# Kernel tuning notes

Measured on AMD Instinct MI355X. Metric: run time of the kernel, lower is better.

## Reference

```python
import jax, jax.numpy as jnp
import numpy as np

silu = jax.nn.silu

B, N, E, H, T, L, A = 8, 20000, 40000, 128, 64, 4, 4


def setup_inputs() -> dict:
    key = jax.random.key(0)
    ks = jax.random.split(key, 20)
    s = 0.05
    w = lambda k, shape: jax.random.normal(k, shape, jnp.float32) * s
    return {
        "x": jax.random.normal(ks[0], (B, N, 3), jnp.float32),
        "t": jax.random.uniform(ks[1], (B,), jnp.float32) * 1000.0,
        "atom_types": jax.random.randint(ks[2], (N,), 0, A),
        "bond_indices": jax.random.randint(ks[3], (E, 2), 0, N),
        "emb_table": w(ks[4], (A, H)),
        "W_t1": w(ks[5], (T, H)), "b_t1": jnp.zeros((H,), jnp.float32),
        "W_t2": w(ks[6], (H, H)), "b_t2": jnp.zeros((H,), jnp.float32),
        "W_node": w(ks[7], (H, H)), "b_node": jnp.zeros((H,), jnp.float32),
        "Wm1": w(ks[8], (L, 2 * H + 1, H)), "bm1": jnp.zeros((L, H), jnp.float32),
        "Wm2": w(ks[9], (L, H, H)), "bm2": jnp.zeros((L, H), jnp.float32),
        "Wn1": w(ks[10], (L, 2 * H, H)), "bn1": jnp.zeros((L, H), jnp.float32),
        "Wn2": w(ks[11], (L, H, H)), "bn2": jnp.zeros((L, H), jnp.float32),
        "Wc1": w(ks[12], (L, H, H)), "bc1": jnp.zeros((L, H), jnp.float32),
        "Wc2": w(ks[13], (L, H, 1)) * 0.001,  # xavier gain=0.001 final coord layer
        "W_o1": w(ks[14], (H, H)), "b_o1": jnp.zeros((H,), jnp.float32),
        "W_o2": w(ks[15], (H, 3)), "b_o2": jnp.zeros((3,), jnp.float32),
    }


def reference(x, t, atom_types, bond_indices, emb_table,
              W_t1, b_t1, W_t2, b_t2, W_node, b_node,
              Wm1, bm1, Wm2, bm2, Wn1, bn1, Wn2, bn2, Wc1, bc1, Wc2,
              W_o1, b_o1, W_o2, b_o2):
    n_atoms = x.shape[1]
    src = bond_indices[:, 0]
    dst = bond_indices[:, 1]

    # sinusoidal time embedding -> time MLP
    half = W_t1.shape[0] // 2
    freq = jnp.exp(jnp.arange(half, dtype=jnp.float32) * (-np.log(10000.0) / (half - 1)))
    te = t[:, None] * freq[None, :]
    te = jnp.concatenate([jnp.sin(te), jnp.cos(te)], axis=-1)  # [B, T]
    t_emb = silu(te @ W_t1 + b_t1) @ W_t2 + b_t2  # [B, H]

    # node init: embedding -> linear -> + time emb
    h0 = emb_table[atom_types] @ W_node + b_node  # [N, H]
    h = h0[None, :, :] + t_emb[:, None, :]  # [B, N, H]

    # degree counts (src+dst incidence), clamped to >=1
    ones = jnp.ones((src.shape[0],), jnp.float32)
    counts = jnp.zeros((n_atoms,), jnp.float32).at[dst].add(ones).at[src].add(ones)
    counts = jnp.maximum(counts, 1.0)

    x_orig = x
    n_layers = Wm1.shape[0]
    for l in range(n_layers):
        h_src = h[:, src, :]
        h_dst = h[:, dst, :]
        coord_diff = x[:, dst, :] - x[:, src, :]  # [B, E, 3]
        dist = jnp.sqrt(jnp.sum(coord_diff * coord_diff, axis=-1, keepdims=True))
        msg_in = jnp.concatenate([h_src, h_dst, dist], axis=-1)  # [B, E, 2H+1]
        m = silu(msg_in @ Wm1[l] + bm1[l])
        m = silu(m @ Wm2[l] + bm2[l])  # [B, E, H]

        agg = jnp.zeros_like(h).at[:, dst, :].add(m).at[:, src, :].add(m)
        h_in = jnp.concatenate([h, agg], axis=-1)
        h = h + silu(h_in @ Wn1[l] + bn1[l]) @ Wn2[l] + bn2[l]

        cw = silu(m @ Wc1[l] + bc1[l]) @ Wc2[l]  # [B, E, 1]
        cdn = coord_diff / (dist + 1e-8)
        upd = cdn * cw
        coord_update = jnp.zeros_like(x).at[:, dst, :].add(upd).at[:, src, :].add(-upd)
        x = x + coord_update / counts[None, :, None]

    coord_change = x - x_orig
    noise_from_h = silu(h @ W_o1 + b_o1) @ W_o2 + b_o2
    return coord_change + noise_from_h
```

## Files before the change

### kernel.cpp

```cpp
#include <hip/hip_runtime.h>
#include <math.h>

#define B_ 8
#define N_ 20000
#define E_ 40000
#define H_ 128
#define L_ 4
#define A_ 4
#define TS 132
#define MRS 136
#define EPB 64
#define NPB 64

#define WFENCE __asm__ __volatile__("" ::: "memory")

typedef _Float16 f16x8 __attribute__((ext_vector_type(8)));
typedef _Float16 f16x4v __attribute__((ext_vector_type(4)));
typedef float f32x4 __attribute__((ext_vector_type(4)));

__device__ __forceinline__ float silu_f(float x) {
    return x * __builtin_amdgcn_rcpf(1.f + __expf(-x));
}


__global__ void k_zero(int* __restrict__ deg, int* __restrict__ cursor) {
    int i = blockIdx.x * 256 + threadIdx.x;
    if (i < N_) { deg[i] = 0; cursor[i] = 0; }
}

__global__ void k_deg(const int* __restrict__ bond, int* __restrict__ deg) {
    int e = blockIdx.x * 256 + threadIdx.x;
    if (e < E_) {
        atomicAdd(&deg[bond[2 * e]], 1);
        atomicAdd(&deg[bond[2 * e + 1]], 1);
    }
}

__global__ void k_scan(const int* __restrict__ deg, int* __restrict__ indptr) {
    __shared__ int sums[1024];
    const int CH = (N_ + 1023) / 1024;
    int t = threadIdx.x;
    int s0 = t * CH;
    int s1 = min(s0 + CH, N_);
    int s = 0;
    for (int i = s0; i < s1; ++i) s += deg[i];
    sums[t] = s;
    __syncthreads();
    for (int off = 1; off < 1024; off <<= 1) {
        int v = (t >= off) ? sums[t - off] : 0;
        __syncthreads();
        sums[t] += v;
        __syncthreads();
    }
    int base = (t > 0) ? sums[t - 1] : 0;
    int run = base;
    for (int i = s0; i < s1; ++i) { indptr[i] = run; run += deg[i]; }
    if (s1 == N_ && s0 < N_) indptr[N_] = run;
}

__global__ void k_fill(const int* __restrict__ bond, const int* __restrict__ indptr,
                       int* __restrict__ cursor, int* __restrict__ adj) {
    int e = blockIdx.x * 256 + threadIdx.x;
    if (e < E_) {
        int s = bond[2 * e], d = bond[2 * e + 1];
        int ps = indptr[s] + atomicAdd(&cursor[s], 1);
        adj[ps] = (e << 1);
        int pd = indptr[d] + atomicAdd(&cursor[d], 1);
        adj[pd] = (e << 1) | 1;
    }
}

__global__ void k_wprepL(const float* __restrict__ W, _Float16* __restrict__ Wf,
                         int K, int wstride) {
    int l = blockIdx.y;
    const float* Wl = W + (size_t)l * wstride;
    _Float16* Wfl = Wf + (size_t)l * K * 128;
    int idx = blockIdx.x * 256 + threadIdx.x;
    if (idx >= K * 128) return;
    int j = idx & 7, lane = (idx >> 3) & 63, nt = (idx >> 9) & 7, kt = idx >> 12;
    int k = kt * 32 + (lane >> 4) * 8 + j;
    int n = nt * 16 + (lane & 15);
    Wfl[idx] = (_Float16)Wl[k * 128 + n];
}

__global__ void k_temb(const float* __restrict__ tv,
                       const float* __restrict__ W1, const float* __restrict__ b1,
                       const float* __restrict__ W2, const float* __restrict__ b2,
                       float* __restrict__ t_emb) {
    __shared__ float te[64];
    __shared__ float h1[128];
    int b = blockIdx.x;
    int tid = threadIdx.x;
    float tval = tv[b];
    if (tid < 32) {
        float fr = __expf((float)tid * (-logf(10000.f) / 31.f));
        float a = tval * fr;
        te[tid] = sinf(a);
        te[tid + 32] = cosf(a);
    }
    __syncthreads();
    float acc = b1[tid];
    for (int k = 0; k < 64; ++k) acc += te[k] * W1[k * 128 + tid];
    h1[tid] = silu_f(acc);
    __syncthreads();
    float acc2 = b2[tid];
    for (int k = 0; k < 128; ++k) acc2 += h1[k] * W2[k * 128 + tid];
    t_emb[b * 128 + tid] = acc2;
}

__global__ void k_embproj(const float* __restrict__ emb, const float* __restrict__ W,
                          const float* __restrict__ bias, float* __restrict__ outp) {
    int tid = threadIdx.x;
    int a = tid >> 7, j = tid & 127;
    float acc = bias[j];
    for (int k = 0; k < 128; ++k) acc += emb[a * 128 + k] * W[k * 128 + j];
    outp[a * 128 + j] = acc;
}

__global__ void k_hinit(const int* __restrict__ at, const float* __restrict__ embp,
                        const float* __restrict__ temb, float* __restrict__ h,
                        _Float16* __restrict__ h16) {
    size_t idx4 = (size_t)blockIdx.x * 256 + threadIdx.x;
    size_t e0 = idx4 * 4;
    int j = (int)(e0 % H_);
    size_t bn = e0 / H_;
    int n = (int)(bn % N_);
    int b = (int)(bn / N_);
    int a = at[n];
    float4 ep = *(const float4*)(embp + a * H_ + j);
    float4 tv = *(const float4*)(temb + b * H_ + j);
    float4 r = make_float4(ep.x + tv.x, ep.y + tv.y, ep.z + tv.z, ep.w + tv.w);
    ((float4*)h)[idx4] = r;
    f16x4v o;
    o[0] = (_Float16)r.x; o[1] = (_Float16)r.y; o[2] = (_Float16)r.z; o[3] = (_Float16)r.w;
    *(f16x4v*)(h16 + e0) = o;
}

__global__ void k_xcopy(const float* __restrict__ x, float* __restrict__ xb) {
    int i = blockIdx.x * 256 + threadIdx.x;
    xb[i] = x[i];
}

template <int RS, int KT>
__device__ __forceinline__ void mfma_gemm(const _Float16* Asw, const _Float16* __restrict__ Wf,
                                          f32x4 (&acc)[8], int ml, int quad, int lane) {
    #pragma unroll
    for (int kt = 0; kt < KT; ++kt) {
        f16x8 a = *(const f16x8*)(Asw + ml * RS + kt * 32 + quad * 8);
        #pragma unroll
        for (int nt = 0; nt < 8; ++nt) {
            f16x8 b = *(const f16x8*)(Wf + (((kt * 8 + nt) * 64 + lane) * 8));
            acc[nt] = __builtin_amdgcn_mfma_f32_16x16x32_f16(a, b, acc[nt], 0, 0, 0);
        }
    }
}

template <int RS, int KT>
__device__ __forceinline__ void mfma_gemm2(const _Float16* Asw, const _Float16* __restrict__ Wf,
                                           f32x4 (&acc)[2][8], int ml, int quad, int lane) {
    #pragma unroll
    for (int kt = 0; kt < KT; ++kt) {
        f16x8 a0 = *(const f16x8*)(Asw + ml * RS + kt * 32 + quad * 8);
        f16x8 a1 = *(const f16x8*)(Asw + (16 + ml) * RS + kt * 32 + quad * 8);
        #pragma unroll
        for (int nt = 0; nt < 8; ++nt) {
            f16x8 b = *(const f16x8*)(Wf + (((kt * 8 + nt) * 64 + lane) * 8));
            acc[0][nt] = __builtin_amdgcn_mfma_f32_16x16x32_f16(a0, b, acc[0][nt], 0, 0, 0);
            acc[1][nt] = __builtin_amdgcn_mfma_f32_16x16x32_f16(a1, b, acc[1][nt], 0, 0, 0);
        }
    }
}

template <int STRIDE, int K>
__device__ __forceinline__ void gemm_t(const float* As, const float* __restrict__ W,
                                       float (&acc)[4][8], int r4, int c) {
    const float4* Wv = (const float4*)W;
    #pragma unroll 2
    for (int k = 0; k < K; k += 4) {
        float a[4][4];
        #pragma unroll
        for (int i = 0; i < 4; ++i)
            *(float4*)a[i] = *(const float4*)(As + (r4 + i) * STRIDE + k);
        #pragma unroll
        for (int kk = 0; kk < 4; ++kk) {
            float4 w0 = Wv[(k + kk) * 32 + c * 2];
            float4 w1 = Wv[(k + kk) * 32 + c * 2 + 1];
            #pragma unroll
            for (int i = 0; i < 4; ++i) {
                float av = a[i][kk];
                acc[i][0] += av * w0.x; acc[i][1] += av * w0.y;
                acc[i][2] += av * w0.z; acc[i][3] += av * w0.w;
                acc[i][4] += av * w1.x; acc[i][5] += av * w1.y;
                acc[i][6] += av * w1.z; acc[i][7] += av * w1.w;
            }
        }
    }
}

__device__ __forceinline__ void bias_init(float (&acc)[4][8], const float* __restrict__ bias, int c) {
    float4 b0 = ((const float4*)bias)[c * 2];
    float4 b1 = ((const float4*)bias)[c * 2 + 1];
    #pragma unroll
    for (int i = 0; i < 4; ++i) {
        acc[i][0] = b0.x; acc[i][1] = b0.y; acc[i][2] = b0.z; acc[i][3] = b0.w;
        acc[i][4] = b1.x; acc[i][5] = b1.y; acc[i][6] = b1.z; acc[i][7] = b1.w;
    }
}


__global__ __launch_bounds__(128, 4) void k_edge_mfma(
    const _Float16* __restrict__ h16, const float* __restrict__ xcur,
    const int* __restrict__ bond,
    const float* __restrict__ Wm1, const float* __restrict__ bm1,
    const _Float16* __restrict__ Wm1f,
    const float* __restrict__ bm2, const _Float16* __restrict__ Wm2f,
    const float* __restrict__ bc1, const _Float16* __restrict__ Wc1f,
    const float* __restrict__ Wc2,
    _Float16* __restrict__ m16, float* __restrict__ cw_out) {
    __shared__ _Float16 As[EPB * MRS];
    __shared__ float ds_s[EPB];
    int tid = threadIdx.x;
    int b = blockIdx.x & 7;
    int e0 = (blockIdx.x >> 3) * EPB;
    size_t be0 = (size_t)b * E_ + e0;

    int el = tid >> 1, q = tid & 1;
    int2 sd = ((const int2*)bond)[e0 + el];
    int s = sd.x, d = sd.y;
    if (q == 0) {
        const float* xs = xcur + ((size_t)b * N_ + s) * 3;
        const float* xd = xcur + ((size_t)b * N_ + d) * 3;
        float dx = xd[0] - xs[0], dy = xd[1] - xs[1], dz = xd[2] - xs[2];
        ds_s[el] = sqrtf(dx * dx + dy * dy + dz * dz);
    }
    {
        const _Float16* hs = h16 + ((size_t)b * N_ + s) * H_;
        #pragma unroll
        for (int j = 0; j < 8; ++j)
            *(f16x8*)(As + el * MRS + q * 64 + j * 8) = *(const f16x8*)(hs + q * 64 + j * 8);
    }
    WFENCE;

    int lane = tid & 63, w = tid >> 6;
    int ml = lane & 15, quad = lane >> 4;
    _Float16* Asw = As + w * 32 * MRS;
    const float* wd = Wm1 + 256 * H_;

    f32x4 acc[2][8];
    #pragma unroll
    for (int nt = 0; nt < 8; ++nt) {
        int col = nt * 16 + ml;
        float bb = bm1[col];
        float ww = wd[col];
        #pragma unroll
        for (int rt = 0; rt < 2; ++rt)
            #pragma unroll
            for (int r = 0; r < 4; ++r)
                acc[rt][nt][r] = bb + ds_s[w * 32 + rt * 16 + quad * 4 + r] * ww;
    }
    mfma_gemm2<MRS, 4>(Asw, Wm1f, acc, ml, quad, lane);
    WFENCE;
    {
        const _Float16* hd = h16 + ((size_t)b * N_ + d) * H_;
        #pragma unroll
        for (int j = 0; j < 8; ++j)
            *(f16x8*)(As + el * MRS + q * 64 + j * 8) = *(const f16x8*)(hd + q * 64 + j * 8);
    }
    WFENCE;
    mfma_gemm2<MRS, 4>(Asw, Wm1f + 4 * 8 * 64 * 8, acc, ml, quad, lane);
    WFENCE;
    #pragma unroll
    for (int rt = 0; rt < 2; ++rt)
        #pragma unroll
        for (int nt = 0; nt < 8; ++nt)
            #pragma unroll
            for (int r = 0; r < 4; ++r)
                Asw[(rt * 16 + quad * 4 + r) * MRS + nt * 16 + ml] = (_Float16)silu_f(acc[rt][nt][r]);
    WFENCE;

    #pragma unroll
    for (int nt = 0; nt < 8; ++nt) {
        float bb = bm2[nt * 16 + ml];
        #pragma unroll
        for (int rt = 0; rt < 2; ++rt)
            #pragma unroll
            for (int r = 0; r < 4; ++r) acc[rt][nt][r] = bb;
    }
    mfma_gemm2<MRS, 4>(Asw, Wm2f, acc, ml, quad, lane);
    WFENCE;
    #pragma unroll
    for (int rt = 0; rt < 2; ++rt)
        #pragma unroll
        for (int nt = 0; nt < 8; ++nt)
            #pragma unroll
            for (int r = 0; r < 4; ++r)
                Asw[(rt * 16 + quad * 4 + r) * MRS + nt * 16 + ml] = (_Float16)silu_f(acc[rt][nt][r]);
    WFENCE;
    #pragma unroll
    for (int j = 0; j < 8; ++j)
        *(f16x8*)(m16 + (be0 + el) * H_ + q * 64 + j * 8) =
            *(const f16x8*)(As + el * MRS + q * 64 + j * 8);

    #pragma unroll
    for (int nt = 0; nt < 8; ++nt) {
        float bb = bc1[nt * 16 + ml];
        #pragma unroll
        for (int rt = 0; rt < 2; ++rt)
            #pragma unroll
            for (int r = 0; r < 4; ++r) acc[rt][nt][r] = bb;
    }
    mfma_gemm2<MRS, 4>(Asw, Wc1f, acc, ml, quad, lane);
    float part[2][4] = {{0.f, 0.f, 0.f, 0.f}, {0.f, 0.f, 0.f, 0.f}};
    #pragma unroll
    for (int nt = 0; nt < 8; ++nt) {
        float wv = Wc2[nt * 16 + ml];
        #pragma unroll
        for (int rt = 0; rt < 2; ++rt)
            #pragma unroll
            for (int r = 0; r < 4; ++r) part[rt][r] += silu_f(acc[rt][nt][r]) * wv;
    }
    #pragma unroll
    for (int off = 1; off < 16; off <<= 1)
        #pragma unroll
        for (int rt = 0; rt < 2; ++rt)
            #pragma unroll
            for (int r = 0; r < 4; ++r) part[rt][r] += __shfl_xor(part[rt][r], off, 64);
    if (ml == 0) {
        #pragma unroll
        for (int rt = 0; rt < 2; ++rt)
            #pragma unroll
            for (int r = 0; r < 4; ++r)
                cw_out[be0 + w * 32 + rt * 16 + quad * 4 + r] = part[rt][r];
    }
}

__global__ void k_coord(const float* __restrict__ xcur, float* __restrict__ xnext,
                        const float* __restrict__ cw, const int* __restrict__ bond,
                        const int* __restrict__ indptr, const int* __restrict__ adj) {
    int idx = blockIdx.x * 256 + threadIdx.x;
    int b = idx / N_;
    int n = idx - b * N_;
    const float* xb = xcur + (size_t)b * N_ * 3;
    int p0 = indptr[n], p1 = indptr[n + 1];
    float ax = 0.f, ay = 0.f, az = 0.f;
    for (int p = p0; p < p1; ++p) {
        int a = adj[p];
        int e = a >> 1;
        float sgn = (a & 1) ? 1.f : -1.f;
        int s = bond[2 * e], d = bond[2 * e + 1];
        float dx = xb[d * 3 + 0] - xb[s * 3 + 0];
        float dy = xb[d * 3 + 1] - xb[s * 3 + 1];
        float dz = xb[d * 3 + 2] - xb[s * 3 + 2];
        float dist = sqrtf(dx * dx + dy * dy + dz * dz);
        float w = cw[(size_t)b * E_ + e] * sgn * __builtin_amdgcn_rcpf(dist + 1e-8f);
        ax += dx * w; ay += dy * w; az += dz * w;
    }
    float rcnt = __builtin_amdgcn_rcpf((float)max(p1 - p0, 1));
    xnext[(size_t)idx * 3 + 0] = xb[n * 3 + 0] + ax * rcnt;
    xnext[(size_t)idx * 3 + 1] = xb[n * 3 + 1] + ay * rcnt;
    xnext[(size_t)idx * 3 + 2] = xb[n * 3 + 2] + az * rcnt;
}

__global__ __launch_bounds__(256, 5) void k_node_mfma(
    float* __restrict__ h, _Float16* __restrict__ h16,
    const _Float16* __restrict__ m16,
    const int* __restrict__ indptr, const int* __restrict__ adj,
    const float* __restrict__ bn1, const _Float16* __restrict__ Wn1f,
    const float* __restrict__ bn2, const _Float16* __restrict__ Wn2f) {
    __shared__ _Float16 As[NPB * MRS];
    int tid = threadIdx.x;
    int el = tid >> 2, q = tid & 3;
    int be = blockIdx.x * NPB + el;
    int b = be / N_, n = be - b * N_;
    {
        const _Float16* hr = h16 + (size_t)be * H_;
        #pragma unroll
        for (int j = 0; j < 4; ++j)
            *(f16x8*)(As + el * MRS + q * 32 + j * 8) = *(const f16x8*)(hr + q * 32 + j * 8);
    }
    WFENCE;

    int lane = tid & 63, w = tid >> 6;
    int ml = lane & 15, quad = lane >> 4;
    _Float16* Asw = As + w * 16 * MRS;
    size_t be0 = (size_t)blockIdx.x * NPB;

    f32x4 acc[8];
    #pragma unroll
    for (int nt = 0; nt < 8; ++nt) {
        float bb = bn1[nt * 16 + ml];
        #pragma unroll
        for (int r = 0; r < 4; ++r) acc[nt][r] = bb;
    }
    mfma_gemm<MRS, 4>(Asw, Wn1f, acc, ml, quad, lane);
    WFENCE;
    {
        float ag[4][8];
        #pragma unroll
        for (int j = 0; j < 4; ++j)
            #pragma unroll
            for (int i = 0; i < 8; ++i) ag[j][i] = 0.f;
        int p0 = indptr[n], p1 = indptr[n + 1];
        for (int p = p0; p < p1; ++p) {
            int e = adj[p] >> 1;
            const _Float16* mp = m16 + ((size_t)b * E_ + e) * H_;
            #pragma unroll
            for (int j = 0; j < 4; ++j) {
                f16x8 v = *(const f16x8*)(mp + q * 32 + j * 8);
                #pragma unroll
                for (int i = 0; i < 8; ++i) ag[j][i] += (float)v[i];
            }
        }
        #pragma unroll
        for (int j = 0; j < 4; ++j) {
            f16x8 o;
            #pragma unroll
            for (int i = 0; i < 8; ++i) o[i] = (_Float16)ag[j][i];
            *(f16x8*)(As + el * MRS + q * 32 + j * 8) = o;
        }
    }
    WFENCE;
    mfma_gemm<MRS, 4>(Asw, Wn1f + 4 * 8 * 64 * 8, acc, ml, quad, lane);
    WFENCE;
    #pragma unroll
    for (int nt = 0; nt < 8; ++nt)
        #pragma unroll
        for (int r = 0; r < 4; ++r)
            Asw[(quad * 4 + r) * MRS + nt * 16 + ml] = (_Float16)silu_f(acc[nt][r]);
    WFENCE;
    f32x4 acc2[8];
    #pragma unroll
    for (int nt = 0; nt < 8; ++nt) {
        float bb = bn2[nt * 16 + ml];
        #pragma unroll
        for (int r = 0; r < 4; ++r) acc2[nt][r] = bb;
    }
    mfma_gemm<MRS, 4>(Asw, Wn2f, acc2, ml, quad, lane);
    #pragma unroll
    for (int nt = 0; nt < 8; ++nt)
        #pragma unroll
        for (int r = 0; r < 4; ++r) {
            int row = w * 16 + quad * 4 + r;
            size_t g = (size_t)(be0 + row) * H_ + nt * 16 + ml;
            float v = h[g] + acc2[nt][r];
            h[g] = v;
            h16[g] = (_Float16)v;
        }
}

__global__ __launch_bounds__(256) void k_out2(
    const float* __restrict__ h, const float* __restrict__ xfin, const float* __restrict__ xorig,
    const float* __restrict__ Wo1, const float* __restrict__ bo1,
    const float* __restrict__ Wo2, const float* __restrict__ bo2,
    float* __restrict__ out) {
    __shared__ float As[64 * TS];
    __shared__ float red[64 * 48];
    int tid = threadIdx.x;
    {
        int nl = tid >> 2, q = tid & 3;
        size_t row = (size_t)blockIdx.x * 64 + nl;
        const float4* hr = (const float4*)(h + row * H_);
        #pragma unroll
        for (int j = 0; j < 8; ++j) {
            int f4 = j * 4 + q;
            *(float4*)(As + nl * TS + f4 * 4) = hr[f4];
        }
    }
    __syncthreads();
    int r4 = (tid >> 4) * 4, c = tid & 15;
    float acc[4][8];
    bias_init(acc, bo1, c);
    gemm_t<TS, 128>(As, Wo1, acc, r4, c);
    #pragma unroll
    for (int i = 0; i < 4; ++i) {
        float p0 = 0.f, p1 = 0.f, p2 = 0.f;
        #pragma unroll
        for (int j = 0; j < 8; ++j) {
            float u = silu_f(acc[i][j]);
            int col = c * 8 + j;
            p0 += u * Wo2[col * 3 + 0];
            p1 += u * Wo2[col * 3 + 1];
            p2 += u * Wo2[col * 3 + 2];
        }
        red[(r4 + i) * 48 + c * 3 + 0] = p0;
        red[(r4 + i) * 48 + c * 3 + 1] = p1;
        red[(r4 + i) * 48 + c * 3 + 2] = p2;
    }
    __syncthreads();
    if (tid < 192) {
        int row = tid / 3, jj = tid - row * 3;
        float s = 0.f;
        #pragma unroll
        for (int cc = 0; cc < 16; ++cc) s += red[row * 48 + cc * 3 + jj];
        size_t grow = (size_t)blockIdx.x * 64 + row;
        out[grow * 3 + jj] = s + bo2[jj] + xfin[grow * 3 + jj] - xorig[grow * 3 + jj];
    }
}


extern "C" void kernel_launch(void* const* d_in, const int* in_sizes, int n_in,
                              void* d_out, int out_size, void* d_ws, size_t ws_size,
                              hipStream_t stream) {
    const float* x = (const float*)d_in[0];
    const float* t = (const float*)d_in[1];
    const int* atom_types = (const int*)d_in[2];
    const int* bond = (const int*)d_in[3];
    const float* emb_table = (const float*)d_in[4];
    const float* W_t1 = (const float*)d_in[5];
    const float* b_t1 = (const float*)d_in[6];
    const float* W_t2 = (const float*)d_in[7];
    const float* b_t2 = (const float*)d_in[8];
    const float* W_node = (const float*)d_in[9];
    const float* b_node = (const float*)d_in[10];
    const float* Wm1 = (const float*)d_in[11];
    const float* bm1 = (const float*)d_in[12];
    const float* Wm2 = (const float*)d_in[13];
    const float* bm2 = (const float*)d_in[14];
    const float* Wn1 = (const float*)d_in[15];
    const float* bn1 = (const float*)d_in[16];
    const float* Wn2 = (const float*)d_in[17];
    const float* bn2 = (const float*)d_in[18];
    const float* Wc1 = (const float*)d_in[19];
    const float* bc1 = (const float*)d_in[20];
    const float* Wc2 = (const float*)d_in[21];
    const float* W_o1 = (const float*)d_in[22];
    const float* b_o1 = (const float*)d_in[23];
    const float* W_o2 = (const float*)d_in[24];
    const float* b_o2 = (const float*)d_in[25];
    float* out = (float*)d_out;

    char* p = (char*)d_ws;
    auto alloc = [&](size_t bytes) -> void* {
        void* r = (void*)p;
        p += (bytes + 255) & ~(size_t)255;
        return r;
    };
    float* t_emb = (float*)alloc((size_t)B_ * H_ * 4);
    float* emb_proj = (float*)alloc((size_t)A_ * H_ * 4);
    int* deg = (int*)alloc((size_t)N_ * 4);
    int* indptr = (int*)alloc((size_t)(N_ + 1) * 4);
    int* cursor = (int*)alloc((size_t)N_ * 4);
    int* adj = (int*)alloc((size_t)2 * E_ * 4);
    float* xb0 = (float*)alloc((size_t)B_ * N_ * 3 * 4);
    float* xb1 = (float*)alloc((size_t)B_ * N_ * 3 * 4);
    float* cw = (float*)alloc((size_t)B_ * E_ * 4);
    float* h = (float*)alloc((size_t)B_ * N_ * H_ * 4);
    _Float16* h16 = (_Float16*)alloc((size_t)B_ * N_ * H_ * 2);
    _Float16* m16 = (_Float16*)alloc((size_t)B_ * E_ * H_ * 2);
    _Float16* Wm1f = (_Float16*)alloc((size_t)L_ * 256 * H_ * 2);
    _Float16* Wm2f = (_Float16*)alloc((size_t)L_ * H_ * H_ * 2);
    _Float16* Wc1f = (_Float16*)alloc((size_t)L_ * H_ * H_ * 2);
    _Float16* Wn1f = (_Float16*)alloc((size_t)L_ * 256 * H_ * 2);
    _Float16* Wn2f = (_Float16*)alloc((size_t)L_ * H_ * H_ * 2);

    k_zero<<<(N_ + 255) / 256, 256, 0, stream>>>(deg, cursor);
    k_deg<<<(E_ + 255) / 256, 256, 0, stream>>>(bond, deg);
    k_scan<<<1, 1024, 0, stream>>>(deg, indptr);
    k_fill<<<(E_ + 255) / 256, 256, 0, stream>>>(bond, indptr, cursor, adj);
    k_temb<<<B_, 128, 0, stream>>>(t, W_t1, b_t1, W_t2, b_t2, t_emb);
    k_embproj<<<1, 512, 0, stream>>>(emb_table, W_node, b_node, emb_proj);
    k_hinit<<<(B_ * N_ * H_ / 4) / 256, 256, 0, stream>>>(atom_types, emb_proj, t_emb, h, h16);
    k_xcopy<<<(B_ * N_ * 3) / 256, 256, 0, stream>>>(x, xb0);
    k_wprepL<<<dim3(128, L_), 256, 0, stream>>>(Wm1, Wm1f, 256, 257 * H_);
    k_wprepL<<<dim3(64, L_), 256, 0, stream>>>(Wm2, Wm2f, 128, H_ * H_);
    k_wprepL<<<dim3(64, L_), 256, 0, stream>>>(Wc1, Wc1f, 128, H_ * H_);
    k_wprepL<<<dim3(128, L_), 256, 0, stream>>>(Wn1, Wn1f, 256, 2 * H_ * H_);
    k_wprepL<<<dim3(64, L_), 256, 0, stream>>>(Wn2, Wn2f, 128, H_ * H_);

    float* xc = xb0;
    float* xn = xb1;
    for (int l = 0; l < L_; ++l) {
        k_edge_mfma<<<(B_ * E_) / EPB, 128, 0, stream>>>(
            h16, xc, bond,
            Wm1 + (size_t)l * 257 * H_, bm1 + l * H_, Wm1f + (size_t)l * 256 * H_,
            bm2 + l * H_, Wm2f + (size_t)l * H_ * H_,
            bc1 + l * H_, Wc1f + (size_t)l * H_ * H_,
            Wc2 + (size_t)l * H_, m16, cw);
        k_coord<<<(B_ * N_) / 256, 256, 0, stream>>>(xc, xn, cw, bond, indptr, adj);
        k_node_mfma<<<(B_ * N_) / NPB, 256, 0, stream>>>(
            h, h16, m16, indptr, adj,
            bn1 + l * H_, Wn1f + (size_t)l * 256 * H_,
            bn2 + l * H_, Wn2f + (size_t)l * H_ * H_);
        float* tmp = xc; xc = xn; xn = tmp;
    }
    k_out2<<<(B_ * N_) / 64, 256, 0, stream>>>(h, xc, x, W_o1, b_o1, W_o2, b_o2, out);
}
```

Measured before the change: 1.132 ms.

## Fuse coordinate update into node kernel and prefetch dst features into registers

Removes the separate k_coord launch and computes each node's coordinate update inside k_node_mfma. The incident edges are split across the four threads that already share a node row, and the partial sums are combined with lane shuffles. In the edge kernel, the destination node's h16 row is loaded into registers at kernel start so its global latency overlaps the first GEMM, instead of being loaded after it. This saves one launch and one pass over the adjacency, but adds register pressure in both kernels.

New measurement: 1.408 ms. 24.3% more time.

```diff
diff --git a/kernel.cpp b/kernel.cpp
--- a/kernel.cpp
+++ b/kernel.cpp
@@ -227,6 +227,13 @@
     int el = tid >> 1, q = tid & 1;
     int2 sd = ((const int2*)bond)[e0 + el];
     int s = sd.x, d = sd.y;
+    f16x8 hdreg[8];
+    {
+        const _Float16* hd = h16 + ((size_t)b * N_ + d) * H_;
+        #pragma unroll
+        for (int j = 0; j < 8; ++j)
+            hdreg[j] = *(const f16x8*)(hd + q * 64 + j * 8);
+    }
     if (q == 0) {
         const float* xs = xcur + ((size_t)b * N_ + s) * 3;
         const float* xd = xcur + ((size_t)b * N_ + d) * 3;
@@ -260,12 +267,9 @@
     }
     mfma_gemm2<MRS, 4>(Asw, Wm1f, acc, ml, quad, lane);
     WFENCE;
-    {
-        const _Float16* hd = h16 + ((size_t)b * N_ + d) * H_;
-        #pragma unroll
-        for (int j = 0; j < 8; ++j)
-            *(f16x8*)(As + el * MRS + q * 64 + j * 8) = *(const f16x8*)(hd + q * 64 + j * 8);
-    }
+    #pragma unroll
+    for (int j = 0; j < 8; ++j)
+        *(f16x8*)(As + el * MRS + q * 64 + j * 8) = hdreg[j];
     WFENCE;
     mfma_gemm2<MRS, 4>(Asw, Wm1f + 4 * 8 * 64 * 8, acc, ml, quad, lane);
     WFENCE;
@@ -332,39 +336,15 @@
             for (int r = 0; r < 4; ++r)
                 cw_out[be0 + w * 32 + rt * 16 + quad * 4 + r] = part[rt][r];
     }
-}
-
-__global__ void k_coord(const float* __restrict__ xcur, float* __restrict__ xnext,
-                        const float* __restrict__ cw, const int* __restrict__ bond,
-                        const int* __restrict__ indptr, const int* __restrict__ adj) {
-    int idx = blockIdx.x * 256 + threadIdx.x;
-    int b = idx / N_;
-    int n = idx - b * N_;
-    const float* xb = xcur + (size_t)b * N_ * 3;
-    int p0 = indptr[n], p1 = indptr[n + 1];
-    float ax = 0.f, ay = 0.f, az = 0.f;
-    for (int p = p0; p < p1; ++p) {
-        int a = adj[p];
-        int e = a >> 1;
-        float sgn = (a & 1) ? 1.f : -1.f;
-        int s = bond[2 * e], d = bond[2 * e + 1];
-        float dx = xb[d * 3 + 0] - xb[s * 3 + 0];
-        float dy = xb[d * 3 + 1] - xb[s * 3 + 1];
-        float dz = xb[d * 3 + 2] - xb[s * 3 + 2];
-        float dist = sqrtf(dx * dx + dy * dy + dz * dz);
-        float w = cw[(size_t)b * E_ + e] * sgn * __builtin_amdgcn_rcpf(dist + 1e-8f);
-        ax += dx * w; ay += dy * w; az += dz * w;
-    }
-    float rcnt = __builtin_amdgcn_rcpf((float)max(p1 - p0, 1));
-    xnext[(size_t)idx * 3 + 0] = xb[n * 3 + 0] + ax * rcnt;
-    xnext[(size_t)idx * 3 + 1] = xb[n * 3 + 1] + ay * rcnt;
-    xnext[(size_t)idx * 3 + 2] = xb[n * 3 + 2] + az * rcnt;
 }
 
 __global__ __launch_bounds__(256, 5) void k_node_mfma(
     float* __restrict__ h, _Float16* __restrict__ h16,
     const _Float16* __restrict__ m16,
     const int* __restrict__ indptr, const int* __restrict__ adj,
+    const int* __restrict__ bond,
+    const float* __restrict__ xcur, float* __restrict__ xnext,
+    const float* __restrict__ cw,
     const float* __restrict__ bn1, const _Float16* __restrict__ Wn1f,
     const float* __restrict__ bn2, const _Float16* __restrict__ Wn2f) {
     __shared__ _Float16 As[NPB * MRS];
@@ -372,6 +352,7 @@
     int el = tid >> 2, q = tid & 3;
     int be = blockIdx.x * NPB + el;
     int b = be / N_, n = be - b * N_;
+    const float* xb = xcur + (size_t)b * N_ * 3;
     {
         const _Float16* hr = h16 + (size_t)be * H_;
         #pragma unroll
@@ -394,15 +375,17 @@
     }
     mfma_gemm<MRS, 4>(Asw, Wn1f, acc, ml, quad, lane);
     WFENCE;
+    int p0 = indptr[n], p1 = indptr[n + 1];
+    float ax = 0.f, ay = 0.f, az = 0.f;
     {
         float ag[4][8];
         #pragma unroll
         for (int j = 0; j < 4; ++j)
             #pragma unroll
             for (int i = 0; i < 8; ++i) ag[j][i] = 0.f;
-        int p0 = indptr[n], p1 = indptr[n + 1];
         for (int p = p0; p < p1; ++p) {
-            int e = adj[p] >> 1;
+            int a = adj[p];
+            int e = a >> 1;
             const _Float16* mp = m16 + ((size_t)b * E_ + e) * H_;
             #pragma unroll
             for (int j = 0; j < 4; ++j) {
@@ -410,6 +393,16 @@
                 #pragma unroll
                 for (int i = 0; i < 8; ++i) ag[j][i] += (float)v[i];
             }
+            if (((p - p0) & 3) == q) {
+                float sgn = (a & 1) ? 1.f : -1.f;
+                int2 sd = ((const int2*)bond)[e];
+                float dx = xb[sd.y * 3 + 0] - xb[sd.x * 3 + 0];
+                float dy = xb[sd.y * 3 + 1] - xb[sd.x * 3 + 1];
+                float dz = xb[sd.y * 3 + 2] - xb[sd.x * 3 + 2];
+                float dist = sqrtf(dx * dx + dy * dy + dz * dz);
+                float wgt = cw[(size_t)b * E_ + e] * sgn * __builtin_amdgcn_rcpf(dist + 1e-8f);
+                ax += dx * wgt; ay += dy * wgt; az += dz * wgt;
+            }
         }
         #pragma unroll
         for (int j = 0; j < 4; ++j) {
@@ -418,6 +411,14 @@
             for (int i = 0; i < 8; ++i) o[i] = (_Float16)ag[j][i];
             *(f16x8*)(As + el * MRS + q * 32 + j * 8) = o;
         }
+    }
+    ax += __shfl_xor(ax, 1, 64); ay += __shfl_xor(ay, 1, 64); az += __shfl_xor(az, 1, 64);
+    ax += __shfl_xor(ax, 2, 64); ay += __shfl_xor(ay, 2, 64); az += __shfl_xor(az, 2, 64);
+    if (q == 0) {
+        float rcnt = __builtin_amdgcn_rcpf((float)max(p1 - p0, 1));
+        xnext[(size_t)be * 3 + 0] = xb[n * 3 + 0] + ax * rcnt;
+        xnext[(size_t)be * 3 + 1] = xb[n * 3 + 1] + ay * rcnt;
+        xnext[(size_t)be * 3 + 2] = xb[n * 3 + 2] + az * rcnt;
     }
     WFENCE;
     mfma_gemm<MRS, 4>(Asw, Wn1f + 4 * 8 * 64 * 8, acc, ml, quad, lane);
@@ -576,9 +577,8 @@
             bm2 + l * H_, Wm2f + (size_t)l * H_ * H_,
             bc1 + l * H_, Wc1f + (size_t)l * H_ * H_,
             Wc2 + (size_t)l * H_, m16, cw);
-        k_coord<<<(B_ * N_) / 256, 256, 0, stream>>>(xc, xn, cw, bond, indptr, adj);
         k_node_mfma<<<(B_ * N_) / NPB, 256, 0, stream>>>(
-            h, h16, m16, indptr, adj,
+            h, h16, m16, indptr, adj, bond, xc, xn, cw,
             bn1 + l * H_, Wn1f + (size_t)l * 256 * H_,
             bn2 + l * H_, Wn2f + (size_t)l * H_ * H_);
         float* tmp = xc; xc = xn; xn = tmp;
```

## Fuse coordinate scatter into edge kernel via atomics, replacing CSR gather kernel

Applied to the files above, without the earlier changes.

The edge kernel now keeps the coordinate difference next to the distance in shared memory and scatters the weighted unit-vector update into a per-node accumulator with float atomics, instead of writing per-edge weights for a separate CSR gather kernel. A zeroing kernel and a light update kernel replace the gather kernel, which re-read bonds and positions and recomputed distances. This trades a gather pass for many scattered atomics (six per edge per batch) and makes the floating-point summation order nondeterministic.

After: 1.646 ms. 1.45x slower.

```diff
diff --git a/kernel.cpp b/kernel.cpp
--- a/kernel.cpp
+++ b/kernel.cpp
@@ -141,6 +141,22 @@
     xb[i] = x[i];
 }
 
+__global__ void k_azero(float* __restrict__ accum) {
+    int i = blockIdx.x * 256 + threadIdx.x;
+    accum[i] = 0.f;
+}
+
+__global__ void k_xupd(const float* __restrict__ xcur, float* __restrict__ xnext,
+                       const float* __restrict__ accum, const int* __restrict__ indptr) {
+    int idx = blockIdx.x * 256 + threadIdx.x;
+    int n = idx % N_;
+    float rcnt = __builtin_amdgcn_rcpf((float)max(indptr[n + 1] - indptr[n], 1));
+    size_t o = (size_t)idx * 3;
+    xnext[o + 0] = xcur[o + 0] + accum[o + 0] * rcnt;
+    xnext[o + 1] = xcur[o + 1] + accum[o + 1] * rcnt;
+    xnext[o + 2] = xcur[o + 2] + accum[o + 2] * rcnt;
+}
+
 template <int RS, int KT>
 __device__ __forceinline__ void mfma_gemm(const _Float16* Asw, const _Float16* __restrict__ Wf,
                                           f32x4 (&acc)[8], int ml, int quad, int lane) {
@@ -216,9 +232,9 @@
     const float* __restrict__ bm2, const _Float16* __restrict__ Wm2f,
     const float* __restrict__ bc1, const _Float16* __restrict__ Wc1f,
     const float* __restrict__ Wc2,
-    _Float16* __restrict__ m16, float* __restrict__ cw_out) {
+    _Float16* __restrict__ m16, float* __restrict__ accum) {
     __shared__ _Float16 As[EPB * MRS];
-    __shared__ float ds_s[EPB];
+    __shared__ float4 ds4[EPB];
     int tid = threadIdx.x;
     int b = blockIdx.x & 7;
     int e0 = (blockIdx.x >> 3) * EPB;
@@ -231,7 +247,7 @@
         const float* xs = xcur + ((size_t)b * N_ + s) * 3;
         const float* xd = xcur + ((size_t)b * N_ + d) * 3;
         float dx = xd[0] - xs[0], dy = xd[1] - xs[1], dz = xd[2] - xs[2];
-        ds_s[el] = sqrtf(dx * dx + dy * dy + dz * dz);
+        ds4[el] = make_float4(dx, dy, dz, sqrtf(dx * dx + dy * dy + dz * dz));
     }
     {
         const _Float16* hs = h16 + ((size_t)b * N_ + s) * H_;
@@ -256,7 +272,7 @@
         for (int rt = 0; rt < 2; ++rt)
             #pragma unroll
             for (int r = 0; r < 4; ++r)
-                acc[rt][nt][r] = bb + ds_s[w * 32 + rt * 16 + quad * 4 + r] * ww;
+                acc[rt][nt][r] = bb + ds4[w * 32 + rt * 16 + quad * 4 + r].w * ww;
     }
     mfma_gemm2<MRS, 4>(Asw, Wm1f, acc, ml, quad, lane);
     WFENCE;
@@ -329,36 +345,21 @@
         #pragma unroll
         for (int rt = 0; rt < 2; ++rt)
             #pragma unroll
-            for (int r = 0; r < 4; ++r)
-                cw_out[be0 + w * 32 + rt * 16 + quad * 4 + r] = part[rt][r];
-    }
-}
-
-__global__ void k_coord(const float* __restrict__ xcur, float* __restrict__ xnext,
-                        const float* __restrict__ cw, const int* __restrict__ bond,
-                        const int* __restrict__ indptr, const int* __restrict__ adj) {
-    int idx = blockIdx.x * 256 + threadIdx.x;
-    int b = idx / N_;
-    int n = idx - b * N_;
-    const float* xb = xcur + (size_t)b * N_ * 3;
-    int p0 = indptr[n], p1 = indptr[n + 1];
-    float ax = 0.f, ay = 0.f, az = 0.f;
-    for (int p = p0; p < p1; ++p) {
-        int a = adj[p];
-        int e = a >> 1;
-        float sgn = (a & 1) ? 1.f : -1.f;
-        int s = bond[2 * e], d = bond[2 * e + 1];
-        float dx = xb[d * 3 + 0] - xb[s * 3 + 0];
-        float dy = xb[d * 3 + 1] - xb[s * 3 + 1];
-        float dz = xb[d * 3 + 2] - xb[s * 3 + 2];
-        float dist = sqrtf(dx * dx + dy * dy + dz * dz);
-        float w = cw[(size_t)b * E_ + e] * sgn * __builtin_amdgcn_rcpf(dist + 1e-8f);
-        ax += dx * w; ay += dy * w; az += dz * w;
-    }
-    float rcnt = __builtin_amdgcn_rcpf((float)max(p1 - p0, 1));
-    xnext[(size_t)idx * 3 + 0] = xb[n * 3 + 0] + ax * rcnt;
-    xnext[(size_t)idx * 3 + 1] = xb[n * 3 + 1] + ay * rcnt;
-    xnext[(size_t)idx * 3 + 2] = xb[n * 3 + 2] + az * rcnt;
+            for (int r = 0; r < 4; ++r) {
+                int row = w * 32 + rt * 16 + quad * 4 + r;
+                float4 dd = ds4[row];
+                float wgt = part[rt][r] * __builtin_amdgcn_rcpf(dd.w + 1e-8f);
+                int2 sd2 = ((const int2*)bond)[e0 + row];
+                float* ad_ = accum + ((size_t)b * N_ + sd2.y) * 3;
+                float* as_ = accum + ((size_t)b * N_ + sd2.x) * 3;
+                atomicAdd(ad_ + 0,  dd.x * wgt);
+                atomicAdd(ad_ + 1,  dd.y * wgt);
+                atomicAdd(ad_ + 2,  dd.z * wgt);
+                atomicAdd(as_ + 0, -dd.x * wgt);
+                atomicAdd(as_ + 1, -dd.y * wgt);
+                atomicAdd(as_ + 2, -dd.z * wgt);
+            }
+    }
 }
 
 __global__ __launch_bounds__(256, 5) void k_node_mfma(
@@ -543,7 +544,7 @@
     int* adj = (int*)alloc((size_t)2 * E_ * 4);
     float* xb0 = (float*)alloc((size_t)B_ * N_ * 3 * 4);
     float* xb1 = (float*)alloc((size_t)B_ * N_ * 3 * 4);
-    float* cw = (float*)alloc((size_t)B_ * E_ * 4);
+    float* accum = (float*)alloc((size_t)B_ * N_ * 3 * 4);
     float* h = (float*)alloc((size_t)B_ * N_ * H_ * 4);
     _Float16* h16 = (_Float16*)alloc((size_t)B_ * N_ * H_ * 2);
     _Float16* m16 = (_Float16*)alloc((size_t)B_ * E_ * H_ * 2);
@@ -570,13 +571,14 @@
     float* xc = xb0;
     float* xn = xb1;
     for (int l = 0; l < L_; ++l) {
+        k_azero<<<(B_ * N_ * 3) / 256, 256, 0, stream>>>(accum);
         k_edge_mfma<<<(B_ * E_) / EPB, 128, 0, stream>>>(
             h16, xc, bond,
             Wm1 + (size_t)l * 257 * H_, bm1 + l * H_, Wm1f + (size_t)l * 256 * H_,
             bm2 + l * H_, Wm2f + (size_t)l * H_ * H_,
             bc1 + l * H_, Wc1f + (size_t)l * H_ * H_,
-            Wc2 + (size_t)l * H_, m16, cw);
-        k_coord<<<(B_ * N_) / 256, 256, 0, stream>>>(xc, xn, cw, bond, indptr, adj);
+            Wc2 + (size_t)l * H_, m16, accum);
+        k_xupd<<<(B_ * N_) / 256, 256, 0, stream>>>(xc, xn, accum, indptr);
         k_node_mfma<<<(B_ * N_) / NPB, 256, 0, stream>>>(
             h, h16, m16, indptr, adj,
             bn1 + l * H_, Wn1f + (size_t)l * 256 * H_,
```
